# Performance work log

Measured on AMD Instinct MI355X. Metric: run time of the kernel, lower is better.

Reference implementation:

```python
import jax, jax.numpy as jnp
import numpy as np

N_HEAD = 16
P_MIN, P_MAX = 1e-4, 1e3
V_MIN = 1e-10
SHIFT = 5.0


def setup_inputs() -> dict:
    key = jax.random.key(0)
    ks = jax.random.split(key, 4)
    B, T, C = 2, 2048, 1024
    x = jax.random.normal(ks[0], (B, T, C), dtype=jnp.float32)
    w_attn = jax.random.normal(ks[1], (C, 3 * C), dtype=jnp.float32) * 0.02
    b_attn = jnp.zeros((3 * C,), dtype=jnp.float32)
    w_proj = jax.random.normal(ks[2], (C, C), dtype=jnp.float32) * 0.02
    b_proj = jnp.zeros((C,), dtype=jnp.float32)
    p_param = jnp.ones((C,), dtype=jnp.float32)
    return {"x": x, "w_attn": w_attn, "b_attn": b_attn,
            "w_proj": w_proj, "b_proj": b_proj, "p_param": p_param}


def reference(x, w_attn, b_attn, w_proj, b_proj, p_param):
    B, T, C = x.shape
    H = N_HEAD
    d = C // H

    qkv = x @ w_attn + b_attn                      # [B,T,3C]
    q, k, v = jnp.split(qkv, 3, axis=2)

    # signed, clamped power exponent per channel: (sign(p)+0.5).sign() * clamp(|p|)
    p = jnp.sign(jnp.sign(p_param) + 0.5) * jnp.clip(jnp.abs(p_param), P_MIN, P_MAX)

    # log-power transform of V with max-subtraction over T for stability
    v = jnp.clip(jnp.abs(v + SHIFT), V_MIN, None)  # [B,T,C]
    z = p * jnp.log(v)
    z_max = jnp.max(z, axis=1, keepdims=True)      # [B,1,C]
    v = jnp.exp(z - z_max)

    # heads: [B,H,T,d]
    q = q.reshape(B, T, H, d).transpose(0, 2, 1, 3)
    k = k.reshape(B, T, H, d).transpose(0, 2, 1, 3)
    v = v.reshape(B, T, H, d).transpose(0, 2, 1, 3)

    scale = 1.0 / jnp.sqrt(jnp.float32(d))
    scores = jnp.einsum('bhqd,bhkd->bhqk', q, k) * scale
    causal = jnp.tril(jnp.ones((T, T), dtype=bool))
    scores = jnp.where(causal, scores, -jnp.inf)
    att = jax.nn.softmax(scores, axis=-1)
    mean = jnp.einsum('bhqk,bhkd->bhqd', att, v)   # [B,H,T,d]
    mean = mean.transpose(0, 2, 1, 3).reshape(B, T, C)

    # invert the log-power transform (generalized power mean)
    y = jnp.exp((z_max + jnp.log(mean)) / p) - SHIFT
    return y @ w_proj + b_proj
```

## Files before the change

### kernel.cpp

```cpp
#include <hip/hip_runtime.h>
#include <hip/hip_bf16.h>
#include <math.h>

constexpr int B_ = 2;
constexpr int T_ = 2048;
constexpr int C_ = 1024;
constexpr int H_ = 16;
constexpr int D_ = 64;
constexpr int M_ = B_ * T_;
constexpr float SHIFT_ = 5.0f;
constexpr float P_MIN_ = 1e-4f;
constexpr float P_MAX_ = 1e3f;
constexpr float V_MIN_ = 1e-10f;
constexpr float QS_ = 0.125f * 1.4426950408889634f;

typedef __attribute__((ext_vector_type(8))) short s16x8;
typedef __attribute__((ext_vector_type(8))) _Float16 h16x8;
typedef __attribute__((ext_vector_type(4))) float f32x4;
typedef unsigned short ushort_t;

__device__ __forceinline__ float clamp_p(float pp) {
    float s = (pp >= 0.f) ? 1.f : -1.f;
    return s * fminf(fmaxf(fabsf(pp), P_MIN_), P_MAX_);
}

__device__ __forceinline__ ushort_t f2h(float f) {
    _Float16 h = (_Float16)f;
    return __builtin_bit_cast(unsigned short, h);
}
__device__ __forceinline__ float h2f(ushort_t h) {
    return (float)__builtin_bit_cast(_Float16, h);
}

__device__ __forceinline__ float fast_exp2(float x) {
#if __has_builtin(__builtin_amdgcn_exp2f)
    return __builtin_amdgcn_exp2f(x);
#else
    return __expf(x * 0.6931471805599453f);
#endif
}

__device__ __forceinline__ void gload_lds16(const void* g, void* l) {
    __builtin_amdgcn_global_load_lds(
        (const __attribute__((address_space(1))) unsigned int*)g,
        (__attribute__((address_space(3))) unsigned int*)l, 16, 0, 0);
}

__global__ __launch_bounds__(256)
void conv_h(const float* __restrict__ src, ushort_t* __restrict__ hi) {
    int idx = blockIdx.x * 256 + threadIdx.x;
    float4 f = ((const float4*)src)[idx];
    ushort4 h;
    h.x = f2h(f.x); h.y = f2h(f.y); h.z = f2h(f.z); h.w = f2h(f.w);
    ((ushort4*)hi)[idx] = h;
}

__global__ __launch_bounds__(256)
void convT_h(const float* __restrict__ W, ushort_t* __restrict__ Wth,
             int N, int K) {
    __shared__ float tile[64][65];
    const int k0 = blockIdx.y * 64, n0 = blockIdx.x * 64;
    const int tr = threadIdx.x >> 4;
    const int tc4 = (threadIdx.x & 15) * 4;
#pragma unroll
    for (int i = 0; i < 4; ++i) {
        float4 f = *(const float4*)&W[(size_t)(k0 + tr + i * 16) * N + n0 + tc4];
        tile[tr + i * 16][tc4 + 0] = f.x;
        tile[tr + i * 16][tc4 + 1] = f.y;
        tile[tr + i * 16][tc4 + 2] = f.z;
        tile[tr + i * 16][tc4 + 3] = f.w;
    }
    __syncthreads();
#pragma unroll
    for (int i = 0; i < 4; ++i) {
        int n = tr + i * 16;
        ushort4 h;
        h.x = f2h(tile[tc4 + 0][n]);
        h.y = f2h(tile[tc4 + 1][n]);
        h.z = f2h(tile[tc4 + 2][n]);
        h.w = f2h(tile[tc4 + 3][n]);
        *(ushort4*)&Wth[(size_t)(n0 + n) * K + k0 + tc4] = h;
    }
}

template <bool HALF_OUT>
__global__ __launch_bounds__(256)
void gemm1(const ushort_t* __restrict__ Ah, const ushort_t* __restrict__ Bh,
           const float* __restrict__ bias, void* __restrict__ Cout,
           int M, int N, int K, int qcols, float qscale) {
    __shared__ ushort_t Lds[2 * 2 * 128 * 32];

    const int tid = threadIdx.x;
    const int w = tid >> 6;
    const int lane = tid & 63;
    const int l16 = lane & 15;
    const int quad = lane >> 4;
    const int row0 = blockIdx.y * 128, col0 = blockIdx.x * 128;
    const int wr = w >> 1, wc = w & 1;

    const ushort_t* gb[8];
    ushort_t* lb[8];
#pragma unroll
    for (int j = 0; j < 8; ++j) {
        int q = j * 4 + w;
        int plane = q >> 4;
        int cc = q & 15;
        int sub = cc & 1;
        int r = (cc >> 1) * 16 + (lane >> 2);
        const ushort_t* src = plane ? Bh : Ah;
        int tb = plane ? col0 : row0;
        gb[j] = src + (size_t)(tb + r) * K + sub * 32 + (lane & 3) * 8;
        lb[j] = &Lds[plane * 8192 + sub * 4096 + r * 32 + (lane & 3) * 8];
    }

    f32x4 acc[4][4] = {};

    for (int k0 = 0; k0 < K; k0 += 64) {
        __syncthreads();
#pragma unroll
        for (int j = 0; j < 8; ++j)
            gload_lds16(gb[j] + k0, lb[j]);
        __syncthreads();

#pragma unroll
        for (int kk = 0; kk < 2; ++kk) {
            h16x8 af[4], bf[4];
#pragma unroll
            for (int mi = 0; mi < 4; ++mi)
                af[mi] = *(const h16x8*)&Lds[kk * 4096 + (wr * 64 + mi * 16 + l16) * 32 + quad * 8];
#pragma unroll
            for (int ni = 0; ni < 4; ++ni)
                bf[ni] = *(const h16x8*)&Lds[8192 + kk * 4096 + (wc * 64 + ni * 16 + l16) * 32 + quad * 8];
#pragma unroll
            for (int mi = 0; mi < 4; ++mi)
#pragma unroll
                for (int ni = 0; ni < 4; ++ni)
                    acc[mi][ni] = __builtin_amdgcn_mfma_f32_16x16x32_f16(af[mi], bf[ni], acc[mi][ni], 0, 0, 0);
        }
    }

    const float osc = (HALF_OUT && col0 < qcols) ? qscale : 1.0f;

#pragma unroll
    for (int mi = 0; mi < 4; ++mi) {
#pragma unroll
        for (int r = 0; r < 4; ++r) {
            int row = row0 + wr * 64 + mi * 16 + quad * 4 + r;
#pragma unroll
            for (int ni = 0; ni < 4; ++ni) {
                int col = col0 + wc * 64 + ni * 16 + l16;
                float v = acc[mi][ni][r] + bias[col];
                if (HALF_OUT)
                    ((ushort_t*)Cout)[(size_t)row * N + col] = f2h(v * osc);
                else
                    ((float*)Cout)[(size_t)row * N + col] = v;
            }
        }
    }
}

__global__ __launch_bounds__(256)
void zmax_part(const ushort_t* __restrict__ qkvh, const float* __restrict__ p_param,
               float* __restrict__ zpart) {
    const int tch = blockIdx.x & 15;
    const int ctile = (blockIdx.x >> 4) & 15;
    const int b = blockIdx.x >> 8;
    const int col = threadIdx.x & 63;
    const int r = threadIdx.x >> 6;
    const int c = ctile * 64 + col;

    const float p = clamp_p(p_param[c]);
    const ushort_t* vp = qkvh + (size_t)b * T_ * 3 * C_
                       + (size_t)(tch * 128) * 3 * C_ + 2 * C_ + c;

    float lm = -INFINITY;
    for (int t = r; t < 128; t += 4) {
        float v = h2f(vp[(size_t)t * 3 * C_]);
        float z = p * __logf(fmaxf(fabsf(v + SHIFT_), V_MIN_));
        lm = fmaxf(lm, z);
    }
    __shared__ float red[4][64];
    red[r][col] = lm;
    __syncthreads();
    if (threadIdx.x < 64) {
        float m = fmaxf(fmaxf(red[0][threadIdx.x], red[1][threadIdx.x]),
                        fmaxf(red[2][threadIdx.x], red[3][threadIdx.x]));
        zpart[((size_t)b * 16 + tch) * C_ + ctile * 64 + threadIdx.x] = m;
    }
}

__global__ __launch_bounds__(256)
void zmax_fin(const float* __restrict__ zpart, float* __restrict__ zmax) {
    int idx = blockIdx.x * 256 + threadIdx.x;
    int b = idx >> 10;
    int c = idx & (C_ - 1);
    float m = -INFINITY;
#pragma unroll
    for (int ch = 0; ch < 16; ++ch)
        m = fmaxf(m, zpart[((size_t)b * 16 + ch) * C_ + c]);
    zmax[idx] = m;
}

__global__ __launch_bounds__(256)
void prep_kv(const ushort_t* __restrict__ qkvh, const float* __restrict__ p_param,
             const float* __restrict__ zmax,
             ushort_t* __restrict__ kbf, ushort_t* __restrict__ vtbf) {
    __shared__ ushort_t VtL[64 * 72];

    const int blk = blockIdx.x;
    const int tt = blk & 31;
    const int bh = blk >> 5;
    const int b = bh >> 4;
    const int h = bh & 15;
    const int t0 = tt * 64;

    const int tl = threadIdx.x >> 2;
    const int c0 = (threadIdx.x & 3) * 16;
    const int g0 = c0 >> 3;
    const int ptl = ((tl >> 5) & 1) * 32 + ((tl >> 2) & 3) * 8
                  + ((tl >> 4) & 1) * 4 + (tl & 3);

    const size_t rowbase = (size_t)(b * T_ + t0 + tl) * 3 * C_ + h * D_;

    {
        const ushort_t* ksrc = qkvh + rowbase + C_ + c0;
        s16x8 k0v = *(const s16x8*)&ksrc[0];
        s16x8 k1v = *(const s16x8*)&ksrc[8];
        size_t krow = ((size_t)bh * T_ + t0 + tl) * 64;
        *(s16x8*)&kbf[krow + ((g0)     ^ (tl & 7)) * 8] = k0v;
        *(s16x8*)&kbf[krow + ((g0 + 1) ^ (tl & 7)) * 8] = k1v;
    }

    {
        const ushort_t* vsrc = qkvh + rowbase + 2 * C_ + c0;
        ushort_t tv[16];
        *(s16x8*)&tv[0] = *(const s16x8*)&vsrc[0];
        *(s16x8*)&tv[8] = *(const s16x8*)&vsrc[8];
#pragma unroll
        for (int q = 0; q < 16; ++q) {
            int c = h * D_ + c0 + q;
            float p = clamp_p(p_param[c]);
            float v = h2f(tv[q]);
            float z = p * __logf(fmaxf(fabsf(v + SHIFT_), V_MIN_));
            float val = __expf(z - zmax[b * C_ + c]);
            VtL[(c0 + q) * 72 + ptl] = f2h(val);
        }
    }
    __syncthreads();
    {
        const int d = tl;
        s16x8 r0 = *(const s16x8*)&VtL[d * 72 + c0];
        s16x8 r1 = *(const s16x8*)&VtL[d * 72 + c0 + 8];
        size_t vbase = ((size_t)bh * 32 + tt) * 4096 + (size_t)d * 64;
        *(s16x8*)&vtbf[vbase + ((g0)     ^ (d & 7)) * 8] = r0;
        *(s16x8*)&vtbf[vbase + ((g0 + 1) ^ (d & 7)) * 8] = r1;
    }
}

__device__ __forceinline__ void load_frag(h16x8 kf[2][4], const ushort_t* tile,
                                          int l16, int sg0, int sg1) {
#pragma unroll
    for (int nt = 0; nt < 4; ++nt) {
        kf[0][nt] = *(const h16x8*)&tile[(nt * 16 + l16) * 64 + sg0];
        kf[1][nt] = *(const h16x8*)&tile[(nt * 16 + l16) * 64 + sg1];
    }
}

__device__ __forceinline__ void tile_body2(const h16x8 qf[2][2], const h16x8 kf[2][4],
        const h16x8 vf[2][4], const h16x8 ones, bool diag, int l16, int quad, int qh,
        f32x4 O[2][4], f32x4 Ol[2]) {
#pragma unroll
    for (int m = 0; m < 2; ++m) {
        f32x4 s[4] = {};
#pragma unroll
        for (int nt = 0; nt < 4; ++nt) {
            s[nt] = __builtin_amdgcn_mfma_f32_16x16x32_f16(kf[0][nt], qf[m][0], s[nt], 0, 0, 0);
            s[nt] = __builtin_amdgcn_mfma_f32_16x16x32_f16(kf[1][nt], qf[m][1], s[nt], 0, 0, 0);
        }

        if (diag) {
            int row = qh * 32 + m * 16 + l16;
#pragma unroll
            for (int nt = 0; nt < 4; ++nt)
#pragma unroll
                for (int r = 0; r < 4; ++r) {
                    int col = nt * 16 + quad * 4 + r;
                    if (col > row) s[nt][r] = -3.0e38f;
                }
        }

#pragma unroll
        for (int ks = 0; ks < 2; ++ks) {
            ushort_t t8[8];
#pragma unroll
            for (int r = 0; r < 4; ++r) {
                t8[r]     = f2h(fast_exp2(s[2 * ks][r]));
                t8[4 + r] = f2h(fast_exp2(s[2 * ks + 1][r]));
            }
            h16x8 pa = *(const h16x8*)t8;
            Ol[m] = __builtin_amdgcn_mfma_f32_16x16x32_f16(pa, ones, Ol[m], 0, 0, 0);
#pragma unroll
            for (int nt = 0; nt < 4; ++nt)
                O[m][nt] = __builtin_amdgcn_mfma_f32_16x16x32_f16(pa, vf[ks][nt], O[m][nt], 0, 0, 0);
        }
    }
}

__global__ __launch_bounds__(256, 2)
void attn_mfma(const ushort_t* __restrict__ qkvh,
               const ushort_t* __restrict__ kbf, const ushort_t* __restrict__ vtbf,
               float* __restrict__ obuf, float* __restrict__ ml) {
    __shared__ float Osum[2][32][65];
    __shared__ float Lsum[2][32];

    const int tid = threadIdx.x;
    const int w = tid >> 6;
    const int lane = tid & 63;
    const int l16 = lane & 15;
    const int quad = lane >> 4;
    const int qh = w >> 1;
    const int kp = w & 1;

    const int qt = 31 - (blockIdx.x >> 5);
    const int bh = blockIdx.x & 31;
    const int b = bh >> 4;
    const int h = bh & 15;
    const int q0 = qt * 64;

    const int sg0 = ((0 + quad) ^ (l16 & 7)) * 8;
    const int sg1 = ((4 + quad) ^ (l16 & 7)) * 8;

    f32x4 O[2][4] = {};
    f32x4 Ol[2] = {};

    h16x8 ones;
#pragma unroll
    for (int i = 0; i < 8; ++i) ones[i] = (_Float16)1.0f;

    h16x8 qf[2][2];
#pragma unroll
    for (int m = 0; m < 2; ++m) {
        const int qrow = q0 + qh * 32 + m * 16 + l16;
        const ushort_t* qrp = qkvh + (size_t)(b * T_ + qrow) * 3 * C_ + h * D_;
#pragma unroll
        for (int ks = 0; ks < 2; ++ks)
            qf[m][ks] = *(const h16x8*)&qrp[ks * 32 + quad * 8];
    }

    const ushort_t* khead = kbf + (size_t)bh * T_ * 64;
    const ushort_t* vhead = vtbf + (size_t)bh * 32 * 4096;

    if (kp <= qt) {
        h16x8 kfA[2][4], kfB[2][4], vfA[2][4], vfB[2][4];
        load_frag(kfA, khead + (size_t)kp * 4096, l16, sg0, sg1);
        load_frag(vfA, vhead + (size_t)kp * 4096, l16, sg0, sg1);

        for (int kt = kp; kt <= qt; kt += 4) {
            int ktB = (kt + 2 <= qt) ? kt + 2 : kt;
            load_frag(kfB, khead + (size_t)ktB * 4096, l16, sg0, sg1);
            load_frag(vfB, vhead + (size_t)ktB * 4096, l16, sg0, sg1);
            tile_body2(qf, kfA, vfA, ones, kt == qt, l16, quad, qh, O, Ol);
            if (kt + 2 > qt) break;
            int ktA = (kt + 4 <= qt) ? kt + 4 : kt + 2;
            load_frag(kfA, khead + (size_t)ktA * 4096, l16, sg0, sg1);
            load_frag(vfA, vhead + (size_t)ktA * 4096, l16, sg0, sg1);
            tile_body2(qf, kfB, vfB, ones, kt + 2 == qt, l16, quad, qh, O, Ol);
        }
    }

    if (kp == 0) {
#pragma unroll
        for (int m = 0; m < 2; ++m)
#pragma unroll
            for (int r = 0; r < 4; ++r) {
                int lr = m * 16 + quad * 4 + r;
#pragma unroll
                for (int nt = 0; nt < 4; ++nt)
                    Osum[qh][lr][nt * 16 + l16] = O[m][nt][r];
                if (l16 == 0) Lsum[qh][lr] = Ol[m][r];
            }
    }
    __syncthreads();
    if (kp == 1) {
#pragma unroll
        for (int m = 0; m < 2; ++m)
#pragma unroll
            for (int r = 0; r < 4; ++r) {
                int lr = m * 16 + quad * 4 + r;
                int t = q0 + qh * 32 + lr;
                float* dst = obuf + (size_t)(b * T_ + t) * C_ + h * D_;
#pragma unroll
                for (int nt = 0; nt < 4; ++nt)
                    dst[nt * 16 + l16] = O[m][nt][r] + Osum[qh][lr][nt * 16 + l16];
                if (l16 == 0)
                    ml[bh * T_ + t] = Ol[m][r] + Lsum[qh][lr];
            }
    }
}

__global__ __launch_bounds__(256)
void combine_y(const float* __restrict__ obuf, const float* __restrict__ p_param,
               const float* __restrict__ zmax, const float* __restrict__ ml,
               ushort_t* __restrict__ yh) {
    int idx = blockIdx.x * 256 + threadIdx.x;
    int n4 = idx * 4;
    int c = n4 & (C_ - 1);
    int bt = n4 >> 10;
    int t = bt & (T_ - 1);
    int b = bt >> 11;
    int h = c >> 6;
    int bh = b * H_ + h;

    float inv_den = 1.f / ml[bh * T_ + t];

    float4 O0 = *(const float4*)&obuf[(size_t)bt * C_ + c];
    float4 zm = *(const float4*)&zmax[b * C_ + c];
    float4 pp = *(const float4*)&p_param[c];

    ushort4 hh;
    {
        float mean = O0.x * inv_den;
        float y = __expf((zm.x + __logf(mean)) / clamp_p(pp.x)) - SHIFT_;
        hh.x = f2h(y);
    }
    {
        float mean = O0.y * inv_den;
        float y = __expf((zm.y + __logf(mean)) / clamp_p(pp.y)) - SHIFT_;
        hh.y = f2h(y);
    }
    {
        float mean = O0.z * inv_den;
        float y = __expf((zm.z + __logf(mean)) / clamp_p(pp.z)) - SHIFT_;
        hh.z = f2h(y);
    }
    {
        float mean = O0.w * inv_den;
        float y = __expf((zm.w + __logf(mean)) / clamp_p(pp.w)) - SHIFT_;
        hh.w = f2h(y);
    }
    ((ushort4*)yh)[idx] = hh;
}

extern "C" void kernel_launch(void* const* d_in, const int* in_sizes, int n_in,
                              void* d_out, int out_size, void* d_ws, size_t ws_size,
                              hipStream_t stream) {
    const float* x      = (const float*)d_in[0];
    const float* w_attn = (const float*)d_in[1];
    const float* b_attn = (const float*)d_in[2];
    const float* w_proj = (const float*)d_in[3];
    const float* b_proj = (const float*)d_in[4];
    const float* p_par  = (const float*)d_in[5];
    float* out = (float*)d_out;

    char* ws = (char*)d_ws;
    ushort_t* qkvh = (ushort_t*)ws;
    ushort_t* xh   = qkvh + (size_t)M_ * 3 * C_;
    ushort_t* wth  = xh + (size_t)M_ * C_;
    float* obuf = (float*)(wth + (size_t)3 * C_ * C_);
    float* zmax = obuf + (size_t)M_ * C_;
    ushort_t* kbf  = (ushort_t*)(zmax + B_ * C_);
    ushort_t* vtbf = kbf + (size_t)B_ * H_ * T_ * 64;
    float* ml = (float*)(vtbf + (size_t)B_ * H_ * T_ * 64);
    float* zpart = ml + 32 * T_;

    conv_h<<<M_ * C_ / 1024, 256, 0, stream>>>(x, xh);
    convT_h<<<dim3(3 * C_ / 64, C_ / 64), 256, 0, stream>>>(w_attn, wth, 3 * C_, C_);
    gemm1<true><<<dim3(3 * C_ / 128, M_ / 128), 256, 0, stream>>>(
        xh, wth, b_attn, qkvh, M_, 3 * C_, C_, C_, QS_);
    zmax_part<<<B_ * 16 * 16, 256, 0, stream>>>(qkvh, p_par, zpart);
    zmax_fin<<<B_ * C_ / 256, 256, 0, stream>>>(zpart, zmax);
    prep_kv<<<B_ * H_ * 32, 256, 0, stream>>>(qkvh, p_par, zmax, kbf, vtbf);
    attn_mfma<<<B_ * H_ * (T_ / 64), 256, 0, stream>>>(qkvh, kbf, vtbf, obuf, ml);
    combine_y<<<M_ * C_ / 1024, 256, 0, stream>>>(obuf, p_par, zmax, ml, xh);
    convT_h<<<dim3(C_ / 64, C_ / 64), 256, 0, stream>>>(w_proj, wth, C_, C_);
    gemm1<false><<<dim3(C_ / 128, M_ / 128), 256, 0, stream>>>(
        xh, wth, b_proj, out, M_, C_, C_, 0, 1.0f);
}
```

Before: 223.5 us.

## Fuse conversion kernels, zmax finalize, and output combine into neighboring kernels

```diff
diff --git a/kernel.cpp b/kernel.cpp
--- a/kernel.cpp
+++ b/kernel.cpp
@@ -46,22 +46,13 @@
         (__attribute__((address_space(3))) unsigned int*)l, 16, 0, 0);
 }
 
-__global__ __launch_bounds__(256)
-void conv_h(const float* __restrict__ src, ushort_t* __restrict__ hi) {
-    int idx = blockIdx.x * 256 + threadIdx.x;
-    float4 f = ((const float4*)src)[idx];
-    ushort4 h;
-    h.x = f2h(f.x); h.y = f2h(f.y); h.z = f2h(f.z); h.w = f2h(f.w);
-    ((ushort4*)hi)[idx] = h;
-}
-
-__global__ __launch_bounds__(256)
-void convT_h(const float* __restrict__ W, ushort_t* __restrict__ Wth,
-             int N, int K) {
-    __shared__ float tile[64][65];
-    const int k0 = blockIdx.y * 64, n0 = blockIdx.x * 64;
-    const int tr = threadIdx.x >> 4;
-    const int tc4 = (threadIdx.x & 15) * 4;
+__device__ __forceinline__ void convT_body(const float* __restrict__ W,
+                                           ushort_t* __restrict__ Wth,
+                                           int N, int K, int bx, int by,
+                                           int tid, float (*tile)[65]) {
+    const int k0 = by * 64, n0 = bx * 64;
+    const int tr = tid >> 4;
+    const int tc4 = (tid & 15) * 4;
 #pragma unroll
     for (int i = 0; i < 4; ++i) {
         float4 f = *(const float4*)&W[(size_t)(k0 + tr + i * 16) * N + n0 + tc4];
@@ -80,6 +71,28 @@
         h.z = f2h(tile[tc4 + 2][n]);
         h.w = f2h(tile[tc4 + 3][n]);
         *(ushort4*)&Wth[(size_t)(n0 + n) * K + k0 + tc4] = h;
+    }
+}
+
+__global__ __launch_bounds__(256)
+void prep_w(const float* __restrict__ x, const float* __restrict__ w_attn,
+            const float* __restrict__ w_proj, ushort_t* __restrict__ xh,
+            ushort_t* __restrict__ wth, ushort_t* __restrict__ wtp) {
+    __shared__ float tile[64][65];
+    const int blk = blockIdx.x;
+    const int tid = threadIdx.x;
+    if (blk < 4096) {
+        int idx = blk * 256 + tid;
+        float4 f = ((const float4*)x)[idx];
+        ushort4 h;
+        h.x = f2h(f.x); h.y = f2h(f.y); h.z = f2h(f.z); h.w = f2h(f.w);
+        ((ushort4*)xh)[idx] = h;
+    } else if (blk < 4096 + 768) {
+        int sub = blk - 4096;
+        convT_body(w_attn, wth, 3 * C_, C_, sub % 48, sub / 48, tid, tile);
+    } else {
+        int sub = blk - 4864;
+        convT_body(w_proj, wtp, C_, C_, sub % 16, sub / 16, tid, tile);
     }
 }
 
@@ -190,22 +203,11 @@
 }
 
 __global__ __launch_bounds__(256)
-void zmax_fin(const float* __restrict__ zpart, float* __restrict__ zmax) {
-    int idx = blockIdx.x * 256 + threadIdx.x;
-    int b = idx >> 10;
-    int c = idx & (C_ - 1);
-    float m = -INFINITY;
-#pragma unroll
-    for (int ch = 0; ch < 16; ++ch)
-        m = fmaxf(m, zpart[((size_t)b * 16 + ch) * C_ + c]);
-    zmax[idx] = m;
-}
-
-__global__ __launch_bounds__(256)
 void prep_kv(const ushort_t* __restrict__ qkvh, const float* __restrict__ p_param,
-             const float* __restrict__ zmax,
+             const float* __restrict__ zpart, float* __restrict__ zmax,
              ushort_t* __restrict__ kbf, ushort_t* __restrict__ vtbf) {
     __shared__ ushort_t VtL[64 * 72];
+    __shared__ float zm_l[64];
 
     const int blk = blockIdx.x;
     const int tt = blk & 31;
@@ -219,6 +221,17 @@
     const int g0 = c0 >> 3;
     const int ptl = ((tl >> 5) & 1) * 32 + ((tl >> 2) & 3) * 8
                   + ((tl >> 4) & 1) * 4 + (tl & 3);
+
+    if (threadIdx.x < 64) {
+        int c = h * D_ + threadIdx.x;
+        float m = -INFINITY;
+#pragma unroll
+        for (int ch = 0; ch < 16; ++ch)
+            m = fmaxf(m, zpart[((size_t)b * 16 + ch) * C_ + c]);
+        zm_l[threadIdx.x] = m;
+        zmax[b * C_ + c] = m;
+    }
+    __syncthreads();
 
     const size_t rowbase = (size_t)(b * T_ + t0 + tl) * 3 * C_ + h * D_;
 
@@ -238,12 +251,12 @@
         *(s16x8*)&tv[8] = *(const s16x8*)&vsrc[8];
 #pragma unroll
         for (int q = 0; q < 16; ++q) {
-            int c = h * D_ + c0 + q;
-            float p = clamp_p(p_param[c]);
+            int j = c0 + q;
+            float p = clamp_p(p_param[h * D_ + j]);
             float v = h2f(tv[q]);
             float z = p * __logf(fmaxf(fabsf(v + SHIFT_), V_MIN_));
-            float val = __expf(z - zmax[b * C_ + c]);
-            VtL[(c0 + q) * 72 + ptl] = f2h(val);
+            float val = __expf(z - zm_l[j]);
+            VtL[j * 72 + ptl] = f2h(val);
         }
     }
     __syncthreads();
@@ -309,9 +322,11 @@
 __global__ __launch_bounds__(256, 2)
 void attn_mfma(const ushort_t* __restrict__ qkvh,
                const ushort_t* __restrict__ kbf, const ushort_t* __restrict__ vtbf,
-               float* __restrict__ obuf, float* __restrict__ ml) {
+               const float* __restrict__ zmax, const float* __restrict__ p_param,
+               ushort_t* __restrict__ yh) {
     __shared__ float Osum[2][32][65];
     __shared__ float Lsum[2][32];
+    __shared__ float zm_l[64], ip_l[64];
 
     const int tid = threadIdx.x;
     const int w = tid >> 6;
@@ -326,6 +341,12 @@
     const int b = bh >> 4;
     const int h = bh & 15;
     const int q0 = qt * 64;
+
+    if (tid < 64) {
+        int c = h * D_ + tid;
+        zm_l[tid] = zmax[b * C_ + c];
+        ip_l[tid] = 1.f / clamp_p(p_param[c]);
+    }
 
     const int sg0 = ((0 + quad) ^ (l16 & 7)) * 8;
     const int sg1 = ((4 + quad) ^ (l16 & 7)) * 8;
@@ -388,57 +409,17 @@
             for (int r = 0; r < 4; ++r) {
                 int lr = m * 16 + quad * 4 + r;
                 int t = q0 + qh * 32 + lr;
-                float* dst = obuf + (size_t)(b * T_ + t) * C_ + h * D_;
-#pragma unroll
-                for (int nt = 0; nt < 4; ++nt)
-                    dst[nt * 16 + l16] = O[m][nt][r] + Osum[qh][lr][nt * 16 + l16];
-                if (l16 == 0)
-                    ml[bh * T_ + t] = Ol[m][r] + Lsum[qh][lr];
+                float inv_den = 1.f / (Ol[m][r] + Lsum[qh][lr]);
+                ushort_t* dst = yh + (size_t)(b * T_ + t) * C_ + h * D_;
+#pragma unroll
+                for (int nt = 0; nt < 4; ++nt) {
+                    int col = nt * 16 + l16;
+                    float mean = (O[m][nt][r] + Osum[qh][lr][col]) * inv_den;
+                    float y = __expf((zm_l[col] + __logf(mean)) * ip_l[col]) - SHIFT_;
+                    dst[col] = f2h(y);
+                }
             }
     }
-}
-
-__global__ __launch_bounds__(256)
-void combine_y(const float* __restrict__ obuf, const float* __restrict__ p_param,
-               const float* __restrict__ zmax, const float* __restrict__ ml,
-               ushort_t* __restrict__ yh) {
-    int idx = blockIdx.x * 256 + threadIdx.x;
-    int n4 = idx * 4;
-    int c = n4 & (C_ - 1);
-    int bt = n4 >> 10;
-    int t = bt & (T_ - 1);
-    int b = bt >> 11;
-    int h = c >> 6;
-    int bh = b * H_ + h;
-
-    float inv_den = 1.f / ml[bh * T_ + t];
-
-    float4 O0 = *(const float4*)&obuf[(size_t)bt * C_ + c];
-    float4 zm = *(const float4*)&zmax[b * C_ + c];
-    float4 pp = *(const float4*)&p_param[c];
-
-    ushort4 hh;
-    {
-        float mean = O0.x * inv_den;
-        float y = __expf((zm.x + __logf(mean)) / clamp_p(pp.x)) - SHIFT_;
-        hh.x = f2h(y);
-    }
-    {
-        float mean = O0.y * inv_den;
-        float y = __expf((zm.y + __logf(mean)) / clamp_p(pp.y)) - SHIFT_;
-        hh.y = f2h(y);
-    }
-    {
-        float mean = O0.z * inv_den;
-        float y = __expf((zm.z + __logf(mean)) / clamp_p(pp.z)) - SHIFT_;
-        hh.z = f2h(y);
-    }
-    {
-        float mean = O0.w * inv_den;
-        float y = __expf((zm.w + __logf(mean)) / clamp_p(pp.w)) - SHIFT_;
-        hh.w = f2h(y);
-    }
-    ((ushort4*)yh)[idx] = hh;
 }
 
 extern "C" void kernel_launch(void* const* d_in, const int* in_sizes, int n_in,
@@ -456,23 +437,19 @@
     ushort_t* qkvh = (ushort_t*)ws;
     ushort_t* xh   = qkvh + (size_t)M_ * 3 * C_;
     ushort_t* wth  = xh + (size_t)M_ * C_;
-    float* obuf = (float*)(wth + (size_t)3 * C_ * C_);
-    float* zmax = obuf + (size_t)M_ * C_;
+    ushort_t* wtp  = wth + (size_t)3 * C_ * C_;
+    float* zmax = (float*)(wtp + (size_t)C_ * C_);
     ushort_t* kbf  = (ushort_t*)(zmax + B_ * C_);
     ushort_t* vtbf = kbf + (size_t)B_ * H_ * T_ * 64;
-    float* ml = (float*)(vtbf + (size_t)B_ * H_ * T_ * 64);
-    float* zpart = ml + 32 * T_;
-
-    conv_h<<<M_ * C_ / 1024, 256, 0, stream>>>(x, xh);
-    convT_h<<<dim3(3 * C_ / 64, C_ / 64), 256, 0, stream>>>(w_attn, wth, 3 * C_, C_);
+    float* zpart = (float*)(vtbf + (size_t)B_ * H_ * T_ * 64);
+
+    prep_w<<<4096 + 768 + 256, 256, 0, stream>>>(x, w_attn, w_proj, xh, wth, wtp);
     gemm1<true><<<dim3(3 * C_ / 128, M_ / 128), 256, 0, stream>>>(
         xh, wth, b_attn, qkvh, M_, 3 * C_, C_, C_, QS_);
     zmax_part<<<B_ * 16 * 16, 256, 0, stream>>>(qkvh, p_par, zpart);
-    zmax_fin<<<B_ * C_ / 256, 256, 0, stream>>>(zpart, zmax);
-    prep_kv<<<B_ * H_ * 32, 256, 0, stream>>>(qkvh, p_par, zmax, kbf, vtbf);
-    attn_mfma<<<B_ * H_ * (T_ / 64), 256, 0, stream>>>(qkvh, kbf, vtbf, obuf, ml);
-    combine_y<<<M_ * C_ / 1024, 256, 0, stream>>>(obuf, p_par, zmax, ml, xh);
-    convT_h<<<dim3(C_ / 64, C_ / 64), 256, 0, stream>>>(w_proj, wth, C_, C_);
+    prep_kv<<<B_ * H_ * 32, 256, 0, stream>>>(qkvh, p_par, zpart, zmax, kbf, vtbf);
+    attn_mfma<<<B_ * H_ * (T_ / 64), 256, 0, stream>>>(qkvh, kbf, vtbf,
+                                                       zmax, p_par, xh);
     gemm1<false><<<dim3(C_ / 128, M_ / 128), 256, 0, stream>>>(
-        xh, wth, b_proj, out, M_, C_, C_, 0, 1.0f);
-}
+        xh, wtp, b_proj, out, M_, C_, C_, 0, 1.0f);
+}
```

Result: slower. 230.6 us (+3.2%).
